# Optimization experiments

Hardware: AMD Instinct MI355X
Metric: run time of the kernel (lower is better)

The kernel has to match this reference:

```python
import jax, jax.numpy as jnp
import numpy as np

B, H, S, D = 2, 16, 2048, 64
NEG_INF = -1e30


def setup_inputs() -> dict:
    key = jax.random.key(0)
    kq, kk, kv = jax.random.split(key, 3)
    one = jnp.ones((1,), dtype=jnp.float32)
    return {
        "q": jax.random.normal(kq, (B, H, S, D), dtype=jnp.float32),
        "k": jax.random.normal(kk, (B, H, S, D), dtype=jnp.float32),
        "v": jax.random.normal(kv, (B, H, S, D), dtype=jnp.float32),
        "d_scale_q": one,
        "d_scale_k": one,
        "d_scale_v": one,
        "q_scale_s": one,
        "q_scale_o": one,
        "d_scale_s": one,
    }


def reference(q, k, v, d_scale_q, d_scale_k, d_scale_v, q_scale_s, q_scale_o, d_scale_s):
    # fp8 fused SDPA math (scales modeled exactly; fp8 rounding omitted in reference)
    scale = 1.0 / jnp.sqrt(jnp.asarray(D, q.dtype))
    qf = q * d_scale_q  # dequantized Q
    kf = k * d_scale_k  # dequantized K
    vf = v * d_scale_v  # dequantized V
    s = jnp.einsum("bhqd,bhkd->bhqk", qf, kf) * scale  # [B,H,S,S]
    # causal mask
    causal = jnp.tril(jnp.ones((S, S), dtype=bool))
    s = jnp.where(causal[None, None], s, NEG_INF)
    p = jax.nn.softmax(s, axis=-1)  # softmax probs
    amax_s = jnp.max(jnp.abs(p))  # amax of softmax output before requant
    # requantize probs (q_scale_s) then dequantize (d_scale_s) for PV matmul
    p_dq = p * (q_scale_s * d_scale_s)
    o_raw = jnp.einsum("bhqk,bhkd->bhqd", p_dq, vf)
    amax_o = jnp.max(jnp.abs(o_raw))  # amax of output before quantization
    o = o_raw * q_scale_o  # quantized-scale output
    return (o, amax_s, amax_o)
```

## Files before the change

### kernel.cpp

```cpp
#include <hip/hip_runtime.h>

#define BB 2
#define HH 16
#define SS 2048
#define DD 64

constexpr int OSIZE = BB * HH * SS * DD;
constexpr float LOG2E = 1.4426950408889634f;

using bf16x8 = __attribute__((ext_vector_type(8))) short;
using bf16x4 = __attribute__((ext_vector_type(4))) short;
using f32x4  = __attribute__((ext_vector_type(4))) float;
using u16x8  = __attribute__((ext_vector_type(8))) unsigned short;
using fl4    = __attribute__((ext_vector_type(4))) float;

#define MFMA16(a, b, c) __builtin_amdgcn_mfma_f32_16x16x16bf16_1k(a, b, c, 0, 0, 0)

__device__ __forceinline__ unsigned short f2bf(float f) {
    unsigned int u = __float_as_uint(f);
    return (unsigned short)((u + 0x7fffu + ((u >> 16) & 1u)) >> 16);
}

__device__ __forceinline__ unsigned int pkbf(float lo, float hi) {
    return __builtin_amdgcn_perm(__float_as_uint(hi), __float_as_uint(lo), 0x07060302u);
}

__device__ __forceinline__ void atomicMaxPosF(float* addr, float v) {
    atomicMax(reinterpret_cast<unsigned int*>(addr), __float_as_uint(v));
}

__global__ __launch_bounds__(256) void prep_kv_kernel(
    const float* __restrict__ k, const float* __restrict__ v,
    const float* __restrict__ dsk, const float* __restrict__ dsv,
    unsigned short* __restrict__ kbf, unsigned short* __restrict__ vtb,
    float* __restrict__ out)
{
    const int t  = threadIdx.x;
    const int s0 = blockIdx.x * 64;
    const int bh = blockIdx.y;
    if (blockIdx.x == 0 && bh == 0 && t < 2) out[OSIZE + t] = 0.0f;

    const size_t base = (size_t)bh * SS * DD;
    const float sck = dsk[0], scv = dsv[0];

    {
        const float* kp = k + base + (size_t)s0 * DD + t * 16;
        unsigned short* ko = kbf + base + (size_t)s0 * DD + t * 16;
        fl4 a0 = ((const fl4*)kp)[0], a1 = ((const fl4*)kp)[1];
        fl4 a2 = ((const fl4*)kp)[2], a3 = ((const fl4*)kp)[3];
        u16x8 o0, o1;
        #pragma unroll
        for (int j = 0; j < 4; ++j) {
            o0[j] = f2bf(a0[j] * sck); o0[j + 4] = f2bf(a1[j] * sck);
            o1[j] = f2bf(a2[j] * sck); o1[j + 4] = f2bf(a3[j] * sck);
        }
        ((u16x8*)ko)[0] = o0; ((u16x8*)ko)[1] = o1;
    }

    __shared__ unsigned short T[64 * 72];
    {
        const int r  = t >> 2;
        const int cb = (t & 3) * 16;
        const fl4* vp = (const fl4*)(v + base + (size_t)(s0 + r) * DD + cb);
        unsigned short tmp[16];
        #pragma unroll
        for (int c = 0; c < 4; ++c) {
            fl4 xx = vp[c];
            #pragma unroll
            for (int j = 0; j < 4; ++j) tmp[c * 4 + j] = f2bf(xx[j] * scv);
        }
        *(u16x8*)&T[r * 72 + cb]     = *(u16x8*)&tmp[0];
        *(u16x8*)&T[r * 72 + cb + 8] = *(u16x8*)&tmp[8];
    }
    __syncthreads();
    {
        const int dr = t >> 2;
        const int sb = (t & 3) * 16;
        unsigned short tmp[16];
        #pragma unroll
        for (int j = 0; j < 16; ++j) tmp[j] = T[(sb + j) * 72 + dr];
        unsigned short* op = vtb + base + (size_t)dr * SS + s0 + sb;
        *(u16x8*)op       = *(u16x8*)&tmp[0];
        *(u16x8*)(op + 8) = *(u16x8*)&tmp[8];
    }
}

__global__ __launch_bounds__(512, 4) void fattn_kernel(
    const float* __restrict__ q,
    const unsigned short* __restrict__ kbf,
    const unsigned short* __restrict__ vtb,
    const float* __restrict__ dsq, const float* __restrict__ qss,
    const float* __restrict__ qso, const float* __restrict__ dss,
    float* __restrict__ out)
{
    const int bh = blockIdx.x;
    const int x  = blockIdx.y;
    const int tid  = threadIdx.x;
    const int wave = tid >> 6;
    const int qh   = wave >> 2;
    const int ks   = wave & 3;
    const int lane = tid & 63;
    const int m16  = lane & 15;
    const int quad = lane >> 4;
    const int m7   = m16 & 7;

    __shared__ __align__(16) unsigned short KV[2][2][64 * 64];
    __shared__ float Lred[2][4][2][16];
    __shared__ float Ered[2][4][2][16];

    const float q_scale = dsq[0] * 0.125f * LOG2E;
    const size_t base = (size_t)bh * SS * DD;
    const unsigned short* kbh = kbf + base;
    const unsigned short* vbh = vtb + base;

    const int srow = tid >> 3;
    const int sgc  = (tid & 7) ^ (srow & 7);
    const int koff = srow * DD + sgc * 8;
    const int voff = srow * SS + sgc * 8;
    const int ldso = tid * 8;

    const int gsw0 = (quad ^ m7) * 8;
    const int gsw1 = ((4 | quad) ^ m7) * 8;
    const int krow = (ks * 16 + m16) * 64;
    const int vg   = ks * 2 + (quad >> 1);
    const int vsw  = ((vg ^ m7) * 8) + (quad & 1) * 4;

    const float ss_ = qss[0] * dss[0];
    const float o_q = qso[0];
    float amax_o = 0.0f, amax_s = 0.0f;

    float* Ored = (float*)&KV[0][0][0];

    for (int pass = 0; pass < 2; ++pass) {
        const int qt = pass ? (31 - x) : x;
        const int qb = qt * 64;
        const int nkt = qt + 1;

        bf16x8 qf[2][2];
        #pragma unroll
        for (int nt = 0; nt < 2; ++nt) {
            const float* qp = q + base + (size_t)(qb + qh * 32 + nt * 16 + m16) * DD + quad * 8;
            #pragma unroll
            for (int f = 0; f < 2; ++f) {
                fl4 a = *(const fl4*)(qp + f * 32);
                fl4 b2 = *(const fl4*)(qp + f * 32 + 4);
                #pragma unroll
                for (int j = 0; j < 4; ++j) {
                    qf[nt][f][j]     = (short)f2bf(a[j] * q_scale);
                    qf[nt][f][j + 4] = (short)f2bf(b2[j] * q_scale);
                }
            }
        }

        f32x4 Oacc[4][2];
        #pragma unroll
        for (int dt = 0; dt < 4; ++dt)
            #pragma unroll
            for (int nt = 0; nt < 2; ++nt)
                #pragma unroll
                for (int r = 0; r < 4; ++r) Oacc[dt][nt][r] = 0.0f;
        float l_l[2] = {0.0f, 0.0f}, e_m[2] = {0.0f, 0.0f};

        {
            u16x8 kk = *(const u16x8*)(kbh + koff);
            u16x8 vv = *(const u16x8*)(vbh + voff);
            *(u16x8*)&KV[0][0][ldso] = kk;
            *(u16x8*)&KV[1][0][ldso] = vv;
        }
        __syncthreads();

        for (int t = 0; t < nkt; ++t) {
            const int b = t & 1;
            const bool pf = (t + 1 < nkt);

            u16x8 kpf, vpf;
            if (pf) {
                kpf = *(const u16x8*)(kbh + (size_t)(t + 1) * 64 * DD + koff);
                vpf = *(const u16x8*)(vbh + (t + 1) * 64 + voff);
            }

            const unsigned short* Kt = &KV[0][b][0];
            const unsigned short* Vt = &KV[1][b][0];

            bf16x8 kf0 = *(const bf16x8*)&Kt[krow + gsw0];
            bf16x8 kf1 = *(const bf16x8*)&Kt[krow + gsw1];
            f32x4 sacc[2];
            #pragma unroll
            for (int nt = 0; nt < 2; ++nt) {
                f32x4 acc = {0.0f, 0.0f, 0.0f, 0.0f};
                acc = __builtin_amdgcn_mfma_f32_16x16x32_bf16(kf0, qf[nt][0], acc, 0, 0, 0);
                acc = __builtin_amdgcn_mfma_f32_16x16x32_bf16(kf1, qf[nt][1], acc, 0, 0, 0);
                sacc[nt] = acc;
            }

            if (t == nkt - 1) {
                const int kgb = t * 64 + ks * 16 + quad * 4;
                #pragma unroll
                for (int nt = 0; nt < 2; ++nt) {
                    const int qg = qb + qh * 32 + nt * 16 + m16;
                    #pragma unroll
                    for (int r = 0; r < 4; ++r)
                        if (kgb + r > qg) sacc[nt][r] = -1.0e30f;
                }
            }

            bf16x4 pb[2];
            #pragma unroll
            for (int nt = 0; nt < 2; ++nt) {
                #pragma unroll
                for (int r = 0; r < 4; ++r) {
                    const float e = __builtin_amdgcn_exp2f(sacc[nt][r]);
                    sacc[nt][r] = e;
                    l_l[nt] += e;
                    e_m[nt] = fmaxf(e_m[nt], e);
                }
                union { unsigned int u[2]; bf16x4 h; } cv;
                cv.u[0] = pkbf(sacc[nt][0], sacc[nt][1]);
                cv.u[1] = pkbf(sacc[nt][2], sacc[nt][3]);
                pb[nt] = cv.h;
            }

            #pragma unroll
            for (int dt = 0; dt < 4; ++dt) {
                bf16x4 vf = *(const bf16x4*)&Vt[(dt * 16 + m16) * 64 + vsw];
                #pragma unroll
                for (int nt = 0; nt < 2; ++nt)
                    Oacc[dt][nt] = MFMA16(vf, pb[nt], Oacc[dt][nt]);
            }

            if (pf) {
                *(u16x8*)&KV[0][b ^ 1][ldso] = kpf;
                *(u16x8*)&KV[1][b ^ 1][ldso] = vpf;
            }
            __syncthreads();
        }

        #pragma unroll
        for (int nt = 0; nt < 2; ++nt) {
            l_l[nt] += __shfl_xor(l_l[nt], 16);
            l_l[nt] += __shfl_xor(l_l[nt], 32);
            e_m[nt] = fmaxf(e_m[nt], __shfl_xor(e_m[nt], 16));
            e_m[nt] = fmaxf(e_m[nt], __shfl_xor(e_m[nt], 32));
        }
        if (quad == 0) {
            #pragma unroll
            for (int nt = 0; nt < 2; ++nt) {
                Lred[qh][ks][nt][m16] = l_l[nt];
                Ered[qh][ks][nt][m16] = e_m[nt];
            }
        }

        const int lsw = lane * 32;
        if (ks >= 2) {
            const int s = (qh * 2 + (ks - 2)) * 2048;
            #pragma unroll
            for (int i = 0; i < 8; ++i)
                *(f32x4*)&Ored[s + lsw + ((i ^ (lane & 7)) << 2)] = Oacc[i >> 1][i & 1];
        }
        __syncthreads();
        if (ks < 2) {
            const int s = (qh * 2 + ks) * 2048;
            #pragma unroll
            for (int i = 0; i < 8; ++i) {
                f32x4 a = *(const f32x4*)&Ored[s + lsw + ((i ^ (lane & 7)) << 2)];
                #pragma unroll
                for (int r = 0; r < 4; ++r) Oacc[i >> 1][i & 1][r] += a[r];
            }
        }
        if (ks == 1) {
            const int s = (qh * 2 + 1) * 2048;
            #pragma unroll
            for (int i = 0; i < 8; ++i)
                *(f32x4*)&Ored[s + lsw + ((i ^ (lane & 7)) << 2)] = Oacc[i >> 1][i & 1];
        }
        __syncthreads();
        if (ks == 0) {
            const int s = (qh * 2 + 1) * 2048;
            #pragma unroll
            for (int i = 0; i < 8; ++i) {
                f32x4 a = *(const f32x4*)&Ored[s + lsw + ((i ^ (lane & 7)) << 2)];
                #pragma unroll
                for (int r = 0; r < 4; ++r) Oacc[i >> 1][i & 1][r] += a[r];
            }
            #pragma unroll
            for (int nt = 0; nt < 2; ++nt) {
                float lq = Lred[qh][0][nt][m16] + Lred[qh][1][nt][m16]
                         + Lred[qh][2][nt][m16] + Lred[qh][3][nt][m16];
                float eq = fmaxf(fmaxf(Ered[qh][0][nt][m16], Ered[qh][1][nt][m16]),
                                 fmaxf(Ered[qh][2][nt][m16], Ered[qh][3][nt][m16]));
                amax_s = fmaxf(amax_s, eq / lq);
                const float ivl = ss_ / lq;
                float* oprow = out + base + (size_t)(qb + qh * 32 + nt * 16 + m16) * DD + quad * 4;
                #pragma unroll
                for (int dt = 0; dt < 4; ++dt) {
                    f32x4 ov;
                    #pragma unroll
                    for (int r = 0; r < 4; ++r) {
                        const float o_raw = Oacc[dt][nt][r] * ivl;
                        amax_o = fmaxf(amax_o, fabsf(o_raw));
                        ov[r] = o_raw * o_q;
                    }
                    *(f32x4*)(oprow + dt * 16) = ov;
                }
            }
        }
        __syncthreads();
    }

    if (ks == 0) {
        #pragma unroll
        for (int m = 1; m < 64; m <<= 1) {
            amax_o = fmaxf(amax_o, __shfl_xor(amax_o, m));
            amax_s = fmaxf(amax_s, __shfl_xor(amax_s, m));
        }
        if (lane == 0) {
            atomicMaxPosF(out + OSIZE,     amax_s);
            atomicMaxPosF(out + OSIZE + 1, amax_o);
        }
    }
}

extern "C" void kernel_launch(void* const* d_in, const int* in_sizes, int n_in,
                              void* d_out, int out_size, void* d_ws, size_t ws_size,
                              hipStream_t stream) {
    const float* q   = (const float*)d_in[0];
    const float* k   = (const float*)d_in[1];
    const float* v   = (const float*)d_in[2];
    const float* dsq = (const float*)d_in[3];
    const float* dsk = (const float*)d_in[4];
    const float* dsv = (const float*)d_in[5];
    const float* qss = (const float*)d_in[6];
    const float* qso = (const float*)d_in[7];
    const float* dss = (const float*)d_in[8];
    float* out = (float*)d_out;

    unsigned short* kbf = (unsigned short*)d_ws;
    unsigned short* vtb = (unsigned short*)d_ws + OSIZE;

    prep_kv_kernel<<<dim3(SS / 64, BB * HH), 256, 0, stream>>>(k, v, dsk, dsv, kbf, vtb, out);

    dim3 grid(BB * HH, 16);
    fattn_kernel<<<grid, 512, 0, stream>>>(q, kbf, vtb, dsq, qss, qso, dss, out);
}
```

Before: 163.3 us.

## Widen K/V tile to 128 keys per iteration to halve barrier count

Each loop iteration now stages 128 keys of K and V in shared memory instead of 64, with each wave handling two 16-key subtiles. The goal is to halve the number of __syncthreads barriers and loop iterations, and to issue more MFMAs between barriers. The cost is double the LDS footprint, more live registers for prefetch and scores, and extra masked work when the causal diagonal tile covers an odd number of 64-key blocks.

```diff
diff --git a/kernel.cpp b/kernel.cpp
--- a/kernel.cpp
+++ b/kernel.cpp
@@ -104,7 +104,8 @@
     const int quad = lane >> 4;
     const int m7   = m16 & 7;
 
-    __shared__ __align__(16) unsigned short KV[2][2][64 * 64];
+    __shared__ __align__(16) unsigned short Ksh[2][128 * 64];
+    __shared__ __align__(16) unsigned short Vsh[2][64 * 128];
     __shared__ float Lred[2][4][2][16];
     __shared__ float Ered[2][4][2][16];
 
@@ -113,28 +114,37 @@
     const unsigned short* kbh = kbf + base;
     const unsigned short* vbh = vtb + base;
 
-    const int srow = tid >> 3;
-    const int sgc  = (tid & 7) ^ (srow & 7);
-    const int koff = srow * DD + sgc * 8;
-    const int voff = srow * SS + sgc * 8;
-    const int ldso = tid * 8;
+    const int ksrow = tid >> 2;
+    const int kg0   = (tid & 3) * 2;
+    const int ksrc0 = ksrow * DD + (kg0 ^ (ksrow & 7)) * 8;
+    const int ksrc1 = ksrow * DD + ((kg0 + 1) ^ (ksrow & 7)) * 8;
+    const int klds0 = ksrow * 64 + kg0 * 8;
+    const int vsrow = tid >> 3;
+    const int vg0   = (tid & 7) * 2;
+    const int vsrc0 = vsrow * SS + ((vg0 & 8) | ((vg0 & 7) ^ (vsrow & 7))) * 8;
+    const int vsrc1 = vsrow * SS + (((vg0 + 1) & 8) | (((vg0 + 1) & 7) ^ (vsrow & 7))) * 8;
+    const int vlds0 = vsrow * 128 + vg0 * 8;
 
     const int gsw0 = (quad ^ m7) * 8;
     const int gsw1 = ((4 | quad) ^ m7) * 8;
-    const int krow = (ks * 16 + m16) * 64;
-    const int vg   = ks * 2 + (quad >> 1);
-    const int vsw  = ((vg ^ m7) * 8) + (quad & 1) * 4;
+    int vswk[2];
+    #pragma unroll
+    for (int kt = 0; kt < 2; ++kt) {
+        const int g = ks * 4 + kt * 2 + (quad >> 1);
+        vswk[kt] = ((g & 8) | ((g & 7) ^ m7)) * 8 + (quad & 1) * 4;
+    }
 
     const float ss_ = qss[0] * dss[0];
     const float o_q = qso[0];
     float amax_o = 0.0f, amax_s = 0.0f;
 
-    float* Ored = (float*)&KV[0][0][0];
+    float* Ored = (float*)&Ksh[0][0];
 
     for (int pass = 0; pass < 2; ++pass) {
         const int qt = pass ? (31 - x) : x;
         const int qb = qt * 64;
-        const int nkt = qt + 1;
+        const int nk64 = qt + 1;
+        const int n128 = (nk64 + 1) >> 1;
 
         bf16x8 qf[2][2];
         #pragma unroll
@@ -162,75 +172,94 @@
         float l_l[2] = {0.0f, 0.0f}, e_m[2] = {0.0f, 0.0f};
 
         {
-            u16x8 kk = *(const u16x8*)(kbh + koff);
-            u16x8 vv = *(const u16x8*)(vbh + voff);
-            *(u16x8*)&KV[0][0][ldso] = kk;
-            *(u16x8*)&KV[1][0][ldso] = vv;
+            *(u16x8*)&Ksh[0][klds0]     = *(const u16x8*)(kbh + ksrc0);
+            *(u16x8*)&Ksh[0][klds0 + 8] = *(const u16x8*)(kbh + ksrc1);
+            *(u16x8*)&Vsh[0][vlds0]     = *(const u16x8*)(vbh + vsrc0);
+            *(u16x8*)&Vsh[0][vlds0 + 8] = *(const u16x8*)(vbh + vsrc1);
         }
         __syncthreads();
 
-        for (int t = 0; t < nkt; ++t) {
+        for (int t = 0; t < n128; ++t) {
             const int b = t & 1;
-            const bool pf = (t + 1 < nkt);
-
-            u16x8 kpf, vpf;
+            const bool pf = (t + 1 < n128);
+
+            u16x8 kpf0, kpf1, vpf0, vpf1;
             if (pf) {
-                kpf = *(const u16x8*)(kbh + (size_t)(t + 1) * 64 * DD + koff);
-                vpf = *(const u16x8*)(vbh + (t + 1) * 64 + voff);
-            }
-
-            const unsigned short* Kt = &KV[0][b][0];
-            const unsigned short* Vt = &KV[1][b][0];
-
-            bf16x8 kf0 = *(const bf16x8*)&Kt[krow + gsw0];
-            bf16x8 kf1 = *(const bf16x8*)&Kt[krow + gsw1];
-            f32x4 sacc[2];
-            #pragma unroll
-            for (int nt = 0; nt < 2; ++nt) {
-                f32x4 acc = {0.0f, 0.0f, 0.0f, 0.0f};
-                acc = __builtin_amdgcn_mfma_f32_16x16x32_bf16(kf0, qf[nt][0], acc, 0, 0, 0);
-                acc = __builtin_amdgcn_mfma_f32_16x16x32_bf16(kf1, qf[nt][1], acc, 0, 0, 0);
-                sacc[nt] = acc;
-            }
-
-            if (t == nkt - 1) {
-                const int kgb = t * 64 + ks * 16 + quad * 4;
+                const unsigned short* kg = kbh + (size_t)(t + 1) * 128 * DD;
+                const unsigned short* vg = vbh + (t + 1) * 128;
+                kpf0 = *(const u16x8*)(kg + ksrc0);
+                kpf1 = *(const u16x8*)(kg + ksrc1);
+                vpf0 = *(const u16x8*)(vg + vsrc0);
+                vpf1 = *(const u16x8*)(vg + vsrc1);
+            }
+
+            const unsigned short* Kt = &Ksh[b][0];
+            const unsigned short* Vt = &Vsh[b][0];
+
+            f32x4 sacc[2][2];
+            #pragma unroll
+            for (int kt = 0; kt < 2; ++kt) {
+                const int rb = (ks * 32 + kt * 16 + m16) * 64;
+                bf16x8 kf0 = *(const bf16x8*)&Kt[rb + gsw0];
+                bf16x8 kf1 = *(const bf16x8*)&Kt[rb + gsw1];
                 #pragma unroll
                 for (int nt = 0; nt < 2; ++nt) {
-                    const int qg = qb + qh * 32 + nt * 16 + m16;
+                    f32x4 acc = {0.0f, 0.0f, 0.0f, 0.0f};
+                    acc = __builtin_amdgcn_mfma_f32_16x16x32_bf16(kf0, qf[nt][0], acc, 0, 0, 0);
+                    acc = __builtin_amdgcn_mfma_f32_16x16x32_bf16(kf1, qf[nt][1], acc, 0, 0, 0);
+                    sacc[kt][nt] = acc;
+                }
+            }
+
+            if (t == n128 - 1) {
+                #pragma unroll
+                for (int kt = 0; kt < 2; ++kt) {
+                    const int kgb = t * 128 + ks * 32 + kt * 16 + quad * 4;
                     #pragma unroll
-                    for (int r = 0; r < 4; ++r)
-                        if (kgb + r > qg) sacc[nt][r] = -1.0e30f;
-                }
-            }
-
-            bf16x4 pb[2];
-            #pragma unroll
-            for (int nt = 0; nt < 2; ++nt) {
-                #pragma unroll
-                for (int r = 0; r < 4; ++r) {
-                    const float e = __builtin_amdgcn_exp2f(sacc[nt][r]);
-                    sacc[nt][r] = e;
-                    l_l[nt] += e;
-                    e_m[nt] = fmaxf(e_m[nt], e);
-                }
-                union { unsigned int u[2]; bf16x4 h; } cv;
-                cv.u[0] = pkbf(sacc[nt][0], sacc[nt][1]);
-                cv.u[1] = pkbf(sacc[nt][2], sacc[nt][3]);
-                pb[nt] = cv.h;
-            }
+                    for (int nt = 0; nt < 2; ++nt) {
+                        const int qg = qb + qh * 32 + nt * 16 + m16;
+                        #pragma unroll
+                        for (int r = 0; r < 4; ++r)
+                            if (kgb + r > qg) sacc[kt][nt][r] = -1.0e30f;
+                    }
+                }
+            }
+
+            bf16x4 pb[2][2];
+            #pragma unroll
+            for (int kt = 0; kt < 2; ++kt)
+                #pragma unroll
+                for (int nt = 0; nt < 2; ++nt) {
+                    #pragma unroll
+                    for (int r = 0; r < 4; ++r) {
+                        const float e = __builtin_amdgcn_exp2f(sacc[kt][nt][r]);
+                        sacc[kt][nt][r] = e;
+                        l_l[nt] += e;
+                        e_m[nt] = fmaxf(e_m[nt], e);
+                    }
+                    union { unsigned int u[2]; bf16x4 h; } cv;
+                    cv.u[0] = pkbf(sacc[kt][nt][0], sacc[kt][nt][1]);
+                    cv.u[1] = pkbf(sacc[kt][nt][2], sacc[kt][nt][3]);
+                    pb[kt][nt] = cv.h;
+                }
 
             #pragma unroll
             for (int dt = 0; dt < 4; ++dt) {
-                bf16x4 vf = *(const bf16x4*)&Vt[(dt * 16 + m16) * 64 + vsw];
-                #pragma unroll
-                for (int nt = 0; nt < 2; ++nt)
-                    Oacc[dt][nt] = MFMA16(vf, pb[nt], Oacc[dt][nt]);
+                const int vrow = (dt * 16 + m16) * 128;
+                #pragma unroll
+                for (int kt = 0; kt < 2; ++kt) {
+                    bf16x4 vf = *(const bf16x4*)&Vt[vrow + vswk[kt]];
+                    #pragma unroll
+                    for (int nt = 0; nt < 2; ++nt)
+                        Oacc[dt][nt] = MFMA16(vf, pb[kt][nt], Oacc[dt][nt]);
+                }
             }
 
             if (pf) {
-                *(u16x8*)&KV[0][b ^ 1][ldso] = kpf;
-                *(u16x8*)&KV[1][b ^ 1][ldso] = vpf;
+                *(u16x8*)&Ksh[b ^ 1][klds0]     = kpf0;
+                *(u16x8*)&Ksh[b ^ 1][klds0 + 8] = kpf1;
+                *(u16x8*)&Vsh[b ^ 1][vlds0]     = vpf0;
+                *(u16x8*)&Vsh[b ^ 1][vlds0 + 8] = vpf1;
             }
             __syncthreads();
         }
```

Measured after the change: 176.5 us. +8.1%, slower.

## Split each 64-row query tile across two 256-thread blocks

Applied to the files above, without the earlier changes.

The two query halves of each 64-row tile, previously two wave groups in one 512-thread block, now run as separate 256-thread blocks, doubling the grid to 1024 blocks. Each block loads the full K/V tile itself with two vector loads per thread. This is meant to improve scheduling granularity and occupancy and to shrink barrier scope. The cost is that K/V tiles are now loaded into LDS twice as often, raising global and L2 traffic.

```diff
diff --git a/kernel.cpp b/kernel.cpp
--- a/kernel.cpp
+++ b/kernel.cpp
@@ -85,7 +85,7 @@
     }
 }
 
-__global__ __launch_bounds__(512, 4) void fattn_kernel(
+__global__ __launch_bounds__(256, 4) void fattn_kernel(
     const float* __restrict__ q,
     const unsigned short* __restrict__ kbf,
     const unsigned short* __restrict__ vtb,
@@ -94,19 +94,19 @@
     float* __restrict__ out)
 {
     const int bh = blockIdx.x;
-    const int x  = blockIdx.y;
+    const int x  = blockIdx.y >> 1;
+    const int qh = blockIdx.y & 1;
     const int tid  = threadIdx.x;
-    const int wave = tid >> 6;
-    const int qh   = wave >> 2;
-    const int ks   = wave & 3;
+    const int ks   = tid >> 6;
     const int lane = tid & 63;
     const int m16  = lane & 15;
     const int quad = lane >> 4;
     const int m7   = m16 & 7;
 
-    __shared__ __align__(16) unsigned short KV[2][2][64 * 64];
-    __shared__ float Lred[2][4][2][16];
-    __shared__ float Ered[2][4][2][16];
+    __shared__ __align__(16) unsigned short Ksh[2][64 * 64];
+    __shared__ __align__(16) unsigned short Vsh[2][64 * 64];
+    __shared__ float Lred[4][2][16];
+    __shared__ float Ered[4][2][16];
 
     const float q_scale = dsq[0] * 0.125f * LOG2E;
     const size_t base = (size_t)bh * SS * DD;
@@ -114,10 +114,12 @@
     const unsigned short* vbh = vtb + base;
 
     const int srow = tid >> 3;
-    const int sgc  = (tid & 7) ^ (srow & 7);
-    const int koff = srow * DD + sgc * 8;
-    const int voff = srow * SS + sgc * 8;
-    const int ldso = tid * 8;
+    const int sg   = tid & 7;
+    const int ksrc0 = srow * DD + (sg ^ (srow & 7)) * 8;
+    const int ksrc1 = ksrc0 + 32 * DD;
+    const int vsrc0 = srow * SS + (sg ^ (srow & 7)) * 8;
+    const int vsrc1 = vsrc0 + 32 * SS;
+    const int lds0 = tid * 8, lds1 = (tid + 256) * 8;
 
     const int gsw0 = (quad ^ m7) * 8;
     const int gsw1 = ((4 | quad) ^ m7) * 8;
@@ -129,7 +131,7 @@
     const float o_q = qso[0];
     float amax_o = 0.0f, amax_s = 0.0f;
 
-    float* Ored = (float*)&KV[0][0][0];
+    float* Ored = (float*)&Ksh[0][0];
 
     for (int pass = 0; pass < 2; ++pass) {
         const int qt = pass ? (31 - x) : x;
@@ -162,10 +164,10 @@
         float l_l[2] = {0.0f, 0.0f}, e_m[2] = {0.0f, 0.0f};
 
         {
-            u16x8 kk = *(const u16x8*)(kbh + koff);
-            u16x8 vv = *(const u16x8*)(vbh + voff);
-            *(u16x8*)&KV[0][0][ldso] = kk;
-            *(u16x8*)&KV[1][0][ldso] = vv;
+            *(u16x8*)&Ksh[0][lds0] = *(const u16x8*)(kbh + ksrc0);
+            *(u16x8*)&Ksh[0][lds1] = *(const u16x8*)(kbh + ksrc1);
+            *(u16x8*)&Vsh[0][lds0] = *(const u16x8*)(vbh + vsrc0);
+            *(u16x8*)&Vsh[0][lds1] = *(const u16x8*)(vbh + vsrc1);
         }
         __syncthreads();
 
@@ -173,14 +175,18 @@
             const int b = t & 1;
             const bool pf = (t + 1 < nkt);
 
-            u16x8 kpf, vpf;
+            u16x8 kpf0, kpf1, vpf0, vpf1;
             if (pf) {
-                kpf = *(const u16x8*)(kbh + (size_t)(t + 1) * 64 * DD + koff);
-                vpf = *(const u16x8*)(vbh + (t + 1) * 64 + voff);
-            }
-
-            const unsigned short* Kt = &KV[0][b][0];
-            const unsigned short* Vt = &KV[1][b][0];
+                const unsigned short* kg = kbh + (size_t)(t + 1) * 64 * DD;
+                const unsigned short* vg2 = vbh + (t + 1) * 64;
+                kpf0 = *(const u16x8*)(kg + ksrc0);
+                kpf1 = *(const u16x8*)(kg + ksrc1);
+                vpf0 = *(const u16x8*)(vg2 + vsrc0);
+                vpf1 = *(const u16x8*)(vg2 + vsrc1);
+            }
+
+            const unsigned short* Kt = &Ksh[b][0];
+            const unsigned short* Vt = &Vsh[b][0];
 
             bf16x8 kf0 = *(const bf16x8*)&Kt[krow + gsw0];
             bf16x8 kf1 = *(const bf16x8*)&Kt[krow + gsw1];
@@ -229,8 +235,10 @@
             }
 
             if (pf) {
-                *(u16x8*)&KV[0][b ^ 1][ldso] = kpf;
-                *(u16x8*)&KV[1][b ^ 1][ldso] = vpf;
+                *(u16x8*)&Ksh[b ^ 1][lds0] = kpf0;
+                *(u16x8*)&Ksh[b ^ 1][lds1] = kpf1;
+                *(u16x8*)&Vsh[b ^ 1][lds0] = vpf0;
+                *(u16x8*)&Vsh[b ^ 1][lds1] = vpf1;
             }
             __syncthreads();
         }
@@ -245,21 +253,21 @@
         if (quad == 0) {
             #pragma unroll
             for (int nt = 0; nt < 2; ++nt) {
-                Lred[qh][ks][nt][m16] = l_l[nt];
-                Ered[qh][ks][nt][m16] = e_m[nt];
+                Lred[ks][nt][m16] = l_l[nt];
+                Ered[ks][nt][m16] = e_m[nt];
             }
         }
 
         const int lsw = lane * 32;
         if (ks >= 2) {
-            const int s = (qh * 2 + (ks - 2)) * 2048;
+            const int s = (ks - 2) * 2048;
             #pragma unroll
             for (int i = 0; i < 8; ++i)
                 *(f32x4*)&Ored[s + lsw + ((i ^ (lane & 7)) << 2)] = Oacc[i >> 1][i & 1];
         }
         __syncthreads();
         if (ks < 2) {
-            const int s = (qh * 2 + ks) * 2048;
+            const int s = ks * 2048;
             #pragma unroll
             for (int i = 0; i < 8; ++i) {
                 f32x4 a = *(const f32x4*)&Ored[s + lsw + ((i ^ (lane & 7)) << 2)];
@@ -268,26 +276,24 @@
             }
         }
         if (ks == 1) {
-            const int s = (qh * 2 + 1) * 2048;
             #pragma unroll
             for (int i = 0; i < 8; ++i)
-                *(f32x4*)&Ored[s + lsw + ((i ^ (lane & 7)) << 2)] = Oacc[i >> 1][i & 1];
+                *(f32x4*)&Ored[2048 + lsw + ((i ^ (lane & 7)) << 2)] = Oacc[i >> 1][i & 1];
         }
         __syncthreads();
         if (ks == 0) {
-            const int s = (qh * 2 + 1) * 2048;
             #pragma unroll
             for (int i = 0; i < 8; ++i) {
-                f32x4 a = *(const f32x4*)&Ored[s + lsw + ((i ^ (lane & 7)) << 2)];
+                f32x4 a = *(const f32x4*)&Ored[2048 + lsw + ((i ^ (lane & 7)) << 2)];
                 #pragma unroll
                 for (int r = 0; r < 4; ++r) Oacc[i >> 1][i & 1][r] += a[r];
             }
             #pragma unroll
             for (int nt = 0; nt < 2; ++nt) {
-                float lq = Lred[qh][0][nt][m16] + Lred[qh][1][nt][m16]
-                         + Lred[qh][2][nt][m16] + Lred[qh][3][nt][m16];
-                float eq = fmaxf(fmaxf(Ered[qh][0][nt][m16], Ered[qh][1][nt][m16]),
-                                 fmaxf(Ered[qh][2][nt][m16], Ered[qh][3][nt][m16]));
+                float lq = Lred[0][nt][m16] + Lred[1][nt][m16]
+                         + Lred[2][nt][m16] + Lred[3][nt][m16];
+                float eq = fmaxf(fmaxf(Ered[0][nt][m16], Ered[1][nt][m16]),
+                                 fmaxf(Ered[2][nt][m16], Ered[3][nt][m16]));
                 amax_s = fmaxf(amax_s, eq / lq);
                 const float ivl = ss_ / lq;
                 float* oprow = out + base + (size_t)(qb + qh * 32 + nt * 16 + m16) * DD + quad * 4;
@@ -339,6 +345,6 @@
 
     prep_kv_kernel<<<dim3(SS / 64, BB * HH), 256, 0, stream>>>(k, v, dsk, dsv, kbf, vtb, out);
 
-    dim3 grid(BB * HH, 16);
-    fattn_kernel<<<grid, 512, 0, stream>>>(q, kbf, vtb, dsq, qss, qso, dss, out);
-}
+    dim3 grid(BB * HH, 32);
+    fattn_kernel<<<grid, 256, 0, stream>>>(q, kbf, vtb, dsq, qss, qso, dss, out);
+}
```

New measurement: 175.1 us. 7.2% more time.

## Process two KV tiles per barrier with four-slot shared-memory ring

Applied to the files above, without the earlier changes.

Expands the K/V shared-memory staging from double to quadruple buffering. The loop now handles two key tiles per iteration, prefetching both tiles two steps ahead, so one __syncthreads covers two tiles. This is meant to halve barrier count and deepen the latency hiding of global loads. In exchange LDS use doubles to 64KB, which may cut occupancy, and more registers hold the in-flight prefetches.

```diff
diff --git a/kernel.cpp b/kernel.cpp
--- a/kernel.cpp
+++ b/kernel.cpp
@@ -104,7 +104,8 @@
     const int quad = lane >> 4;
     const int m7   = m16 & 7;
 
-    __shared__ __align__(16) unsigned short KV[2][2][64 * 64];
+    __shared__ __align__(16) unsigned short Ksh[4][64 * 64];
+    __shared__ __align__(16) unsigned short Vsh[4][64 * 64];
     __shared__ float Lred[2][4][2][16];
     __shared__ float Ered[2][4][2][16];
 
@@ -114,9 +115,9 @@
     const unsigned short* vbh = vtb + base;
 
     const int srow = tid >> 3;
-    const int sgc  = (tid & 7) ^ (srow & 7);
-    const int koff = srow * DD + sgc * 8;
-    const int voff = srow * SS + sgc * 8;
+    const int sgc  = ((tid & 7) ^ (srow & 7)) * 8;
+    const int koff = srow * DD + sgc;
+    const int voff = srow * SS + sgc;
     const int ldso = tid * 8;
 
     const int gsw0 = (quad ^ m7) * 8;
@@ -129,7 +130,7 @@
     const float o_q = qso[0];
     float amax_o = 0.0f, amax_s = 0.0f;
 
-    float* Ored = (float*)&KV[0][0][0];
+    float* Ored = (float*)&Ksh[0][0];
 
     for (int pass = 0; pass < 2; ++pass) {
         const int qt = pass ? (31 - x) : x;
@@ -161,27 +162,9 @@
                 for (int r = 0; r < 4; ++r) Oacc[dt][nt][r] = 0.0f;
         float l_l[2] = {0.0f, 0.0f}, e_m[2] = {0.0f, 0.0f};
 
-        {
-            u16x8 kk = *(const u16x8*)(kbh + koff);
-            u16x8 vv = *(const u16x8*)(vbh + voff);
-            *(u16x8*)&KV[0][0][ldso] = kk;
-            *(u16x8*)&KV[1][0][ldso] = vv;
-        }
-        __syncthreads();
-
-        for (int t = 0; t < nkt; ++t) {
-            const int b = t & 1;
-            const bool pf = (t + 1 < nkt);
-
-            u16x8 kpf, vpf;
-            if (pf) {
-                kpf = *(const u16x8*)(kbh + (size_t)(t + 1) * 64 * DD + koff);
-                vpf = *(const u16x8*)(vbh + (t + 1) * 64 + voff);
-            }
-
-            const unsigned short* Kt = &KV[0][b][0];
-            const unsigned short* Vt = &KV[1][b][0];
-
+        auto do_tile = [&](int t, int buf) {
+            const unsigned short* Kt = &Ksh[buf][0];
+            const unsigned short* Vt = &Vsh[buf][0];
             bf16x8 kf0 = *(const bf16x8*)&Kt[krow + gsw0];
             bf16x8 kf1 = *(const bf16x8*)&Kt[krow + gsw1];
             f32x4 sacc[2];
@@ -192,7 +175,6 @@
                 acc = __builtin_amdgcn_mfma_f32_16x16x32_bf16(kf1, qf[nt][1], acc, 0, 0, 0);
                 sacc[nt] = acc;
             }
-
             if (t == nkt - 1) {
                 const int kgb = t * 64 + ks * 16 + quad * 4;
                 #pragma unroll
@@ -203,7 +185,6 @@
                         if (kgb + r > qg) sacc[nt][r] = -1.0e30f;
                 }
             }
-
             bf16x4 pb[2];
             #pragma unroll
             for (int nt = 0; nt < 2; ++nt) {
@@ -219,7 +200,6 @@
                 cv.u[1] = pkbf(sacc[nt][2], sacc[nt][3]);
                 pb[nt] = cv.h;
             }
-
             #pragma unroll
             for (int dt = 0; dt < 4; ++dt) {
                 bf16x4 vf = *(const bf16x4*)&Vt[(dt * 16 + m16) * 64 + vsw];
@@ -227,10 +207,43 @@
                 for (int nt = 0; nt < 2; ++nt)
                     Oacc[dt][nt] = MFMA16(vf, pb[nt], Oacc[dt][nt]);
             }
-
-            if (pf) {
-                *(u16x8*)&KV[0][b ^ 1][ldso] = kpf;
-                *(u16x8*)&KV[1][b ^ 1][ldso] = vpf;
+        };
+
+        {
+            *(u16x8*)&Ksh[0][ldso] = *(const u16x8*)(kbh + koff);
+            *(u16x8*)&Vsh[0][ldso] = *(const u16x8*)(vbh + voff);
+            if (1 < nkt) {
+                *(u16x8*)&Ksh[1][ldso] = *(const u16x8*)(kbh + 64 * DD + koff);
+                *(u16x8*)&Vsh[1][ldso] = *(const u16x8*)(vbh + 64 + voff);
+            }
+        }
+        __syncthreads();
+
+        const int n2 = (nkt + 1) >> 1;
+        for (int j = 0; j < n2; ++j) {
+            const int t0 = 2 * j, t1 = 2 * j + 1;
+            const bool pfa = (t0 + 2 < nkt), pfb = (t1 + 2 < nkt);
+
+            u16x8 ka, va, kb2, vb2;
+            if (pfa) {
+                ka = *(const u16x8*)(kbh + (size_t)(t0 + 2) * 64 * DD + koff);
+                va = *(const u16x8*)(vbh + (t0 + 2) * 64 + voff);
+            }
+            if (pfb) {
+                kb2 = *(const u16x8*)(kbh + (size_t)(t1 + 2) * 64 * DD + koff);
+                vb2 = *(const u16x8*)(vbh + (t1 + 2) * 64 + voff);
+            }
+
+            do_tile(t0, t0 & 3);
+            if (t1 < nkt) do_tile(t1, t1 & 3);
+
+            if (pfa) {
+                *(u16x8*)&Ksh[(t0 + 2) & 3][ldso] = ka;
+                *(u16x8*)&Vsh[(t0 + 2) & 3][ldso] = va;
+            }
+            if (pfb) {
+                *(u16x8*)&Ksh[(t1 + 2) & 3][ldso] = kb2;
+                *(u16x8*)&Vsh[(t1 + 2) & 3][ldso] = vb2;
             }
             __syncthreads();
         }
```

Result: slower. 166.9 us (+2.2%).
